# Kernel tuning notes

Hardware: AMD Instinct MI355X
Metric: run time of the kernel (lower is better)

The kernel has to match this reference:

```python
import jax, jax.numpy as jnp
import numpy as np

HEADS = 4
EPS_LN = 1e-6
EPS_IN = 1e-5


def _ln(x, g, b):
    m = x.mean(-1, keepdims=True)
    v = ((x - m) ** 2).mean(-1, keepdims=True)
    return (x - m) / jnp.sqrt(v + EPS_LN) * g + b


def _inorm(s):
    # nn.InstanceNorm2d(1) (affine=False): normalize each (batch, channel=head)
    # slice over the last two (N, N) dims, biased variance, eps=1e-5.
    m = s.mean((-2, -1), keepdims=True)
    v = ((s - m) ** 2).mean((-2, -1), keepdims=True)
    return (s - m) / jnp.sqrt(v + EPS_IN)


def setup_inputs() -> dict:
    key = jax.random.key(0)
    ks = jax.random.split(key, 32)
    B, C, Hh = 8, 256, HEADS
    sc = 1.0 / np.sqrt(C)

    def n(k, shape, s):
        return jax.random.normal(k, shape, jnp.float32) * s

    return {
        "x": n(ks[0], (B, C, 6, 6, 6), 1.0),
        # global branch params
        "g_tok_w": n(ks[1], (C,), 0.05), "g_tok_b": jnp.zeros((C,), jnp.float32),
        "g_ln1_g": jnp.ones((C,), jnp.float32), "g_ln1_b": jnp.zeros((C,), jnp.float32),
        "g_wq": n(ks[2], (C, C * Hh), sc), "g_wk": n(ks[3], (C, C * Hh), sc),
        "g_wv": n(ks[4], (C, C * Hh), sc), "g_wo": n(ks[5], (C * Hh, C), sc),
        "g_ln2_g": jnp.ones((C,), jnp.float32), "g_ln2_b": jnp.zeros((C,), jnp.float32),
        "g_mo_w": n(ks[6], (C, C), sc), "g_mo_b": jnp.zeros((C,), jnp.float32),
        # local branch params
        "l_pw": n(ks[7], (8, 8), 0.35), "l_pb": jnp.zeros((8,), jnp.float32),
        "l_ln1_g": jnp.ones((C,), jnp.float32), "l_ln1_b": jnp.zeros((C,), jnp.float32),
        "l_wq": n(ks[8], (C, C * Hh), sc), "l_wk": n(ks[9], (C, C * Hh), sc),
        "l_wv": n(ks[10], (C, C * Hh), sc), "l_wo": n(ks[11], (C * Hh, C), sc),
        "l_ln2_g": jnp.ones((C,), jnp.float32), "l_ln2_b": jnp.zeros((C,), jnp.float32),
        "l_mo_w": n(ks[12], (C, C), sc), "l_mo_b": jnp.zeros((C,), jnp.float32),
    }


def _global_branch(x, tok_w, tok_b, ln1_g, ln1_b, wq, wk, wv, wo, ln2_g, ln2_b, mo_w, mo_b):
    B, C, D, H, W = x.shape
    Hh = HEADS
    # TokenLearner_Global: conv1x1x1 (1->256) then mean over (D,H,W), then
    # view(B,C,C).mean(dim=1).  Since the conv is 1x1 on a single input channel,
    # this collapses exactly to: w * mean(x over C,D,H,W) + b.
    m = x.mean((1, 2, 3, 4))                       # (B,)
    tok = m[:, None] * tok_w + tok_b               # (B, C)
    res = tok
    t = _ln(tok, ln1_g, ln1_b)                     # (B, C)
    q = (t @ wq).reshape(B, Hh, C)                 # heads outer in the 1024 split
    k = (t @ wk).reshape(B, Hh, C)
    v = (t @ wv).reshape(B, Hh, C)
    # mh_q^T (B,h,C,1) @ mh_k (B,h,1,C) -> rank-1 (B,h,C,C) score map
    score = q[:, :, :, None] * k[:, :, None, :]
    a = jax.nn.softmax(_inorm(score), axis=-1)
    o = jnp.einsum('bhij,bhj->bhi', a, v)          # attn @ mh_v^T -> (B,h,C)
    # permute(0,3,2,1).view: flatten as (c, heads) with c outer
    o = o.transpose(0, 2, 1).reshape(B, C * Hh)
    out = o @ wo                                   # (B, C)
    tok2 = _ln(out + res, ln2_g, ln2_b)            # (B, C)
    # map_out conv1x1 + GELU on a spatially-constant expand -> compute once
    g = jax.nn.gelu(jnp.einsum('bc,oc->bo', tok2, mo_w) + mo_b, approximate=False)
    return jnp.broadcast_to(g[:, :, None, None, None], (B, C, D, H, W))


def _local_branch(x, pw, pb, ln1_g, ln1_b, wq, wk, wv, wo, ln2_g, ln2_b, mo_w, mo_b):
    B, C, D, H, W = x.shape
    Hh = HEADS
    # TokenLearner_Local: conv3d(1->8, k=2, s=2) per channel == patchify 2x2x2
    xp = x.reshape(B * C, 3, 2, 3, 2, 3, 2).transpose(0, 1, 3, 5, 2, 4, 6)
    xp = xp.reshape(B * C, 27, 8)                  # (BC, patches, patch_vol)
    tok = xp @ pw.T + pb                           # (BC, 27, 8) embed_dim=8
    tok = tok.reshape(B, C, 3, 3, 3, 2, 2, 2)
    # res: (b c)(d h w)(p1 p2 p3) -> b (d p1 h p2 w p3) c
    res = tok.transpose(0, 2, 5, 3, 6, 4, 7, 1).reshape(B, 216, C)
    # attn input: (b c)(d h w)(p1 p2 p3) -> (b d h w) (p1 p2 p3) c
    e = tok.reshape(B, C, 3, 3, 3, 8).transpose(0, 2, 3, 4, 5, 1).reshape(B * 27, 8, C)
    e = _ln(e, ln1_g, ln1_b)
    # (c heads) split: c outer, heads inner
    q = (e @ wq).reshape(B * 27, 8, C, Hh).transpose(0, 3, 2, 1)   # (B27,h,C,8)
    k = (e @ wk).reshape(B * 27, 8, C, Hh).transpose(0, 3, 1, 2)   # (B27,h,8,C)
    v = (e @ wv).reshape(B * 27, 8, C, Hh).transpose(0, 3, 2, 1)   # (B27,h,C,8)
    score = q @ k                                                  # (B27,h,C,C)
    a = jax.nn.softmax(_inorm(score), axis=-1)
    o = a @ v                                                      # (B27,h,C,8)
    # (b d h w) heads c (p1 p2 p3) -> b (d p1 h p2 w p3) (c heads)
    o = o.reshape(B, 3, 3, 3, Hh, C, 2, 2, 2)
    o = o.transpose(0, 1, 6, 2, 7, 3, 8, 5, 4).reshape(B, 216, C * Hh)
    out = o @ wo                                                   # (B,216,C)
    t2 = _ln(out + res, ln2_g, ln2_b)
    xm = t2.transpose(0, 2, 1).reshape(B, C, D, H, W)
    return jax.nn.gelu(
        jnp.einsum('bcdhw,oc->bodhw', xm, mo_w) + mo_b[None, :, None, None, None],
        approximate=False)


def reference(x,
              g_tok_w, g_tok_b, g_ln1_g, g_ln1_b, g_wq, g_wk, g_wv, g_wo,
              g_ln2_g, g_ln2_b, g_mo_w, g_mo_b,
              l_pw, l_pb, l_ln1_g, l_ln1_b, l_wq, l_wk, l_wv, l_wo,
              l_ln2_g, l_ln2_b, l_mo_w, l_mo_b):
    g = _global_branch(x, g_tok_w, g_tok_b, g_ln1_g, g_ln1_b, g_wq, g_wk, g_wv,
                       g_wo, g_ln2_g, g_ln2_b, g_mo_w, g_mo_b)
    l = _local_branch(x, l_pw, l_pb, l_ln1_g, l_ln1_b, l_wq, l_wk, l_wv,
                      l_wo, l_ln2_g, l_ln2_b, l_mo_w, l_mo_b)
    return x + g + l
```

## Files before the change

kernel.cpp:

```cpp
#include <hip/hip_runtime.h>
#include <stdint.h>
#include <math.h>

#define DEVFN __device__ __forceinline__
typedef unsigned short u16;
typedef short bf16x8 __attribute__((ext_vector_type(8)));
typedef float f32x4  __attribute__((ext_vector_type(4)));

DEVFN float blk_sum(float v, float* s4) {
  #pragma unroll
  for (int o = 32; o > 0; o >>= 1) v += __shfl_down(v, o, 64);
  __syncthreads();
  if ((threadIdx.x & 63) == 0) s4[threadIdx.x >> 6] = v;
  __syncthreads();
  return s4[0] + s4[1] + s4[2] + s4[3];
}

DEVFN float gelu_f(float x) {
  return 0.5f * x * (1.f + erff(x * 0.7071067811865475f));
}

DEVFN u16 bf16_rne(float f) {
  uint32_t u = __float_as_uint(f);
  return (u16)((u + 0x7fffu + ((u >> 16) & 1u)) >> 16);
}

DEVFN float bf2f(u16 v) { return __uint_as_float(((uint32_t)v) << 16); }

DEVFN void gload16(const u16* g, u16* l) {
  auto gp = (const __attribute__((address_space(1))) uint32_t*)(uintptr_t)g;
  auto lp = (__attribute__((address_space(3))) uint32_t*)(uintptr_t)l;
  __builtin_amdgcn_global_load_lds(gp, lp, 16, 0, 0);
}

DEVFN void trc_tile(const float* __restrict__ in, u16* __restrict__ out,
                    int R, int C, int r0, int c0, float (*tile)[33], int tid) {
  int tx = tid & 31, ty = tid >> 5;
  for (int i = ty; i < 32; i += 8) tile[i][tx] = in[(size_t)(r0 + i) * C + c0 + tx];
  __syncthreads();
  for (int i = ty; i < 32; i += 8)
    out[(size_t)(c0 + i) * R + r0 + tx] = bf16_rne(tile[tx][i]);
}

__global__ __launch_bounds__(256) void k_l_tok_prep(
    const float* __restrict__ x, const float* __restrict__ pw,
    const float* __restrict__ pb, const float* __restrict__ g1,
    const float* __restrict__ b1, float* __restrict__ res,
    u16* __restrict__ eln_bf, float* __restrict__ g_part,
    const float* __restrict__ wq, const float* __restrict__ wk,
    const float* __restrict__ wv, const float* __restrict__ wo,
    const float* __restrict__ mow, u16* __restrict__ WcatT,
    u16* __restrict__ woT, u16* __restrict__ moB) {
  __shared__ __align__(16) char smem[8448];
  int bid0 = blockIdx.x, tid = threadIdx.x;
  if (bid0 < 1728) {
    float* pws = (float*)smem;
    float* s4 = (float*)(smem + 256);
    int t = bid0;
    int b = t / 216, s = t % 216;
    int z = s / 36, y = (s / 6) % 6, xx = s % 6;
    int d = z >> 1, p1 = z & 1, hh = y >> 1, p2 = y & 1, ww = xx >> 1, p3 = xx & 1;
    int p = p1 * 4 + p2 * 2 + p3;
    int c = tid;
    if (c < 64) pws[c] = pw[c];
    __syncthreads();
    const float* xb = x + (b * 256 + c) * 216 + (2 * d) * 36 + (2 * hh) * 6 + 2 * ww;
    float v = pb[p];
    float xs = 0.f;
    #pragma unroll
    for (int q1 = 0; q1 < 2; ++q1)
      #pragma unroll
      for (int q2 = 0; q2 < 2; ++q2)
        #pragma unroll
        for (int q3 = 0; q3 < 2; ++q3) {
          float xv = xb[q1 * 36 + q2 * 6 + q3];
          xs += xv;
          v += xv * pws[p * 8 + (q1 * 4 + q2 * 2 + q3)];
        }
    float bs = blk_sum(xs, s4);
    if (c == 0) g_part[t] = bs;
    res[t * 256 + c] = v;
    float mu = blk_sum(v, s4) * (1.f / 256.f);
    float dd = v - mu;
    float var = blk_sum(dd * dd, s4) * (1.f / 256.f);
    eln_bf[t * 256 + c] = bf16_rne(dd * rsqrtf(var + 1e-6f) * g1[c] + b1[c]);
  } else {
    float (*tile)[33] = (float(*)[33])smem;
    int bid = bid0 - 1728;
    if (bid < 768) {
      int which = bid >> 8, b2 = bid & 255;
      const float* in = (which == 0) ? wq : (which == 1) ? wk : wv;
      u16* out = WcatT + which * 262144;
      int r0 = (b2 & 7) * 32, c0 = (b2 >> 3) * 32;
      trc_tile(in, out, 256, 1024, r0, c0, tile, tid);
    } else if (bid < 1024) {
      int b2 = bid - 768;
      int r0 = (b2 & 31) * 32, c0 = (b2 >> 5) * 32;
      trc_tile(wo, woT, 1024, 256, r0, c0, tile, tid);
    } else {
      int i = (bid - 1024) * 256 + tid;
      moB[i] = bf16_rne(mow[i]);
    }
  }
}

__global__ __launch_bounds__(256) void k_gemm_qkv_fused(
    const u16* __restrict__ A, const u16* __restrict__ BT, u16* __restrict__ C,
    const float* __restrict__ g_part, const float* __restrict__ tw_,
    const float* __restrict__ tb_, const float* __restrict__ g1,
    const float* __restrict__ b1, const float* __restrict__ wq,
    const float* __restrict__ wk, const float* __restrict__ wv,
    float* __restrict__ gqkv) {
  __shared__ __align__(16) char smem[16640];
  int bid = blockIdx.x, tid = threadIdx.x;
  if (bid < 1296) {
    const int N = 3072, K = 256;
    u16* aL = (u16*)smem;
    u16* bL = (u16*)smem + 2048;
    int rowblk = (bid % 27) * 64, colblk = (bid / 27) * 64;
    int lane = tid & 63, w = tid >> 6;
    int wr = (w >> 1) * 32, wc = (w & 1) * 32;
    int fm = lane & 15, lg = lane >> 4;
    f32x4 acc[2][2] = {};
    for (int kt = 0; kt < K; kt += 32) {
      __syncthreads();
      gload16(&A[(size_t)(rowblk + lane) * K + kt + w * 8], aL + w * 512);
      gload16(&BT[(size_t)(colblk + lane) * K + kt + w * 8], bL + w * 512);
      __syncthreads();
      bf16x8 bn[2];
      #pragma unroll
      for (int ni = 0; ni < 2; ++ni)
        bn[ni] = *(const bf16x8*)&bL[lg * 512 + (wc + ni * 16 + fm) * 8];
      #pragma unroll
      for (int mi = 0; mi < 2; ++mi) {
        bf16x8 af = *(const bf16x8*)&aL[lg * 512 + (wr + mi * 16 + fm) * 8];
        #pragma unroll
        for (int ni = 0; ni < 2; ++ni)
          acc[mi][ni] = __builtin_amdgcn_mfma_f32_16x16x32_bf16(af, bn[ni], acc[mi][ni], 0, 0, 0);
      }
    }
    int crow0 = rowblk + wr + lg * 4;
    int ccol  = colblk + wc + fm;
    #pragma unroll
    for (int mi = 0; mi < 2; ++mi)
      #pragma unroll
      for (int ni = 0; ni < 2; ++ni)
        #pragma unroll
        for (int r = 0; r < 4; ++r)
          C[(size_t)(crow0 + mi * 16 + r) * N + ccol + ni * 16] = bf16_rne(acc[mi][ni][r]);
  } else {
    float* ts = (float*)smem;
    float (*red)[4][8] = (float(*)[4][8])(smem + 8192);
    float* s4 = (float*)(smem + 16384);
    float* m_s = (float*)(smem + 16400);
    int rb = bid - 1296;
    float tw = tw_[tid], tb = tb_[tid], gg = g1[tid], bb = b1[tid];
    float S1 = blk_sum(tw, s4);
    float S2 = blk_sum(tw * tw, s4);
    float S3 = blk_sum(tb, s4);
    float S4 = blk_sum(tb * tb, s4);
    float S5 = blk_sum(tw * tb, s4);
    {
      int b = tid >> 5, sl = tid & 31;
      float a = 0.f;
      for (int k = sl; k < 216; k += 32) a += g_part[b * 216 + k];
      #pragma unroll
      for (int o = 16; o > 0; o >>= 1) a += __shfl_down(a, o, 32);
      if (sl == 0) m_s[b] = a * (1.f / 442368.f);
    }
    __syncthreads();
    #pragma unroll
    for (int b = 0; b < 8; ++b) {
      float m = m_s[b];
      float mu = (m * S1 + S3) * (1.f / 256.f);
      float var = (m * m * S2 + 2.f * m * S5 + S4) * (1.f / 256.f) - mu * mu;
      ts[b * 256 + tid] = (m * tw + tb - mu) * rsqrtf(var + 1e-6f) * gg + bb;
    }
    __syncthreads();
    int col0 = rb * 64;
    int cl = tid & 63, kq = tid >> 6;
    int col = col0 + cl;
    int m = col >> 10, cc = col & 1023;
    const float* W = (m == 0) ? wq : (m == 1) ? wk : wv;
    float acc[8] = {};
    for (int c = kq * 64; c < kq * 64 + 64; ++c) {
      float w = W[c * 1024 + cc];
      #pragma unroll
      for (int b = 0; b < 8; ++b) acc[b] = fmaf(ts[b * 256 + c], w, acc[b]);
    }
    #pragma unroll
    for (int b = 0; b < 8; ++b) red[cl][kq][b] = acc[b];
    __syncthreads();
    if (kq == 0) {
      #pragma unroll
      for (int b = 0; b < 8; ++b)
        gqkv[b * 3072 + col] = red[cl][0][b] + red[cl][1][b] + red[cl][2][b] + red[cl][3][b];
    }
  }
}

__global__ __launch_bounds__(256) void k_l_attn_fused(
    const u16* __restrict__ qkv, u16* __restrict__ o_buf,
    const float* __restrict__ gq, float* __restrict__ g_o) {
  __shared__ __align__(16) uint4 Qb[256], Kb[256];
  __shared__ __align__(16) u16 vt[16][264];
  __shared__ __align__(16) u16 Pl[256][72];
  __shared__ float rqA[64][4], rkA[64][4], rlq[64][4], rlk[64][4], s_ab[2];
  int bid = blockIdx.x, tid = threadIdx.x;
  if (bid >= 864) {
    float* ks = (float*)Qb;
    float* vs = ks + 256;
    float* s4 = (float*)Kb;
    int idx = bid - 864;
    int b = idx >> 2, h = idx & 3;
    int i = tid;
    const float* base = gq + b * 3072 + h * 256;
    float q = base[i];
    float k = base[1024 + i];
    ks[i] = k;
    vs[i] = base[2048 + i];
    float sq  = blk_sum(q, s4);
    float sq2 = blk_sum(q * q, s4);
    float sk  = blk_sum(k, s4);
    float sk2 = blk_sum(k * k, s4);
    float tot  = sq * sk * (1.f / 65536.f);
    float tot2 = sq2 * sk2 * (1.f / 65536.f);
    float rstd = rsqrtf(tot2 - tot * tot + 1e-5f);
    float A = rstd, B = -tot * rstd;
    float den = 0.f, num = 0.f;
    for (int j = 0; j < 256; ++j) {
      float w = __expf(fmaf(q * ks[j], A, B));
      den += w; num += w * vs[j];
    }
    g_o[b * 1024 + (i << 2) + h] = num / den;
    return;
  }
  int n = bid >> 2, h = bid & 3;
  int b = n / 27, patch = n % 27;
  int bz = 2 * (patch / 9), by = 2 * ((patch / 3) % 3), bx = 2 * (patch % 3);
  {
    int c = tid;
    u16 qv[8], kv[8], vv[8];
    #pragma unroll
    for (int p = 0; p < 8; ++p) {
      int t_l = b * 216 + (bz + (p >> 2)) * 36 + (by + ((p >> 1) & 1)) * 6 + (bx + (p & 1));
      const u16* row = qkv + (size_t)t_l * 3072 + (c << 2) + h;
      qv[p] = row[0]; kv[p] = row[1024]; vv[p] = row[2048];
    }
    uint32_t qw[4], kw[4];
    #pragma unroll
    for (int i = 0; i < 4; ++i) {
      qw[i] = (uint32_t)qv[2 * i] | ((uint32_t)qv[2 * i + 1] << 16);
      kw[i] = (uint32_t)kv[2 * i] | ((uint32_t)kv[2 * i + 1] << 16);
    }
    Qb[c] = make_uint4(qw[0], qw[1], qw[2], qw[3]);
    Kb[c] = make_uint4(kw[0], kw[1], kw[2], kw[3]);
    #pragma unroll
    for (int p = 0; p < 8; ++p) vt[p][c] = vv[p];
    vt[8][c] = 0x3F80u;
    #pragma unroll
    for (int r2 = 9; r2 < 16; ++r2) vt[r2][c] = 0;
  }
  __syncthreads();
  {
    int p = tid & 63, chunk = tid >> 6;
    int d = p >> 3, e = p & 7;
    float aq = 0.f, ak = 0.f, lq = 0.f, lk = 0.f;
    for (int cc = chunk * 64; cc < chunk * 64 + 64; ++cc) {
      const u16* qr = (const u16*)&Qb[cc];
      const u16* kr = (const u16*)&Kb[cc];
      float qd = bf2f(qr[d]), qe = bf2f(qr[e]);
      float kd = bf2f(kr[d]), ke = bf2f(kr[e]);
      aq = fmaf(qd, qe, aq); ak = fmaf(kd, ke, ak);
      if (e == 0) { lq += qd; lk += kd; }
    }
    rqA[p][chunk] = aq; rkA[p][chunk] = ak; rlq[p][chunk] = lq; rlk[p][chunk] = lk;
    __syncthreads();
    if (tid < 64) {
      float gq2 = rqA[tid][0] + rqA[tid][1] + rqA[tid][2] + rqA[tid][3];
      float gk = rkA[tid][0] + rkA[tid][1] + rkA[tid][2] + rkA[tid][3];
      float vprod = gq2 * gk, vmu = 0.f;
      if ((tid & 7) == 0) {
        float slq = rlq[tid][0] + rlq[tid][1] + rlq[tid][2] + rlq[tid][3];
        float slk = rlk[tid][0] + rlk[tid][1] + rlk[tid][2] + rlk[tid][3];
        vmu = slq * slk;
      }
      #pragma unroll
      for (int o = 32; o > 0; o >>= 1) {
        vprod += __shfl_down(vprod, o, 64);
        vmu   += __shfl_down(vmu, o, 64);
      }
      if (tid == 0) {
        float mu = vmu * (1.f / 65536.f), m2 = vprod * (1.f / 65536.f);
        float rstd = rsqrtf(m2 - mu * mu + 1e-5f);
        s_ab[0] = rstd; s_ab[1] = -mu * rstd;
      }
    }
    __syncthreads();
  }
  float Af = s_ab[0], Bf = s_ab[1];
  int lane = tid & 63, w = tid >> 6;
  int l15 = lane & 15, lg = lane >> 4;
  bf16x8 qf[4];
  #pragma unroll
  for (int qt = 0; qt < 4; ++qt)
    qf[qt] = *(const bf16x8*)&Qb[w * 64 + qt * 16 + l15];
  f32x4 acc_o[4] = {};
  #pragma unroll 1
  for (int jc = 0; jc < 4; ++jc) {
    bf16x8 kf[4];
    #pragma unroll
    for (int jt = 0; jt < 4; ++jt) {
      bf16x8 z = {};
      if (lg == 0) z = *(const bf16x8*)&Kb[jc * 64 + jt * 16 + l15];
      kf[jt] = z;
    }
    #pragma unroll
    for (int jt = 0; jt < 4; ++jt) {
      #pragma unroll
      for (int qt = 0; qt < 4; ++qt) {
        f32x4 zc = {};
        f32x4 s = __builtin_amdgcn_mfma_f32_16x16x32_bf16(kf[jt], qf[qt], zc, 0, 0, 0);
        float e0 = __expf(fmaf(s[0], Af, Bf));
        float e1 = __expf(fmaf(s[1], Af, Bf));
        float e2 = __expf(fmaf(s[2], Af, Bf));
        float e3 = __expf(fmaf(s[3], Af, Bf));
        uint32_t w0 = (__float_as_uint(e0) >> 16) | (__float_as_uint(e1) & 0xFFFF0000u);
        uint32_t w1 = (__float_as_uint(e2) >> 16) | (__float_as_uint(e3) & 0xFFFF0000u);
        int q = w * 64 + qt * 16 + l15;
        *(uint2*)&Pl[q][jt * 16 + lg * 4] = make_uint2(w0, w1);
      }
    }
    #pragma unroll
    for (int ks2 = 0; ks2 < 2; ++ks2) {
      bf16x8 vf = *(const bf16x8*)&vt[l15][jc * 64 + ks2 * 32 + lg * 8];
      #pragma unroll
      for (int qt = 0; qt < 4; ++qt) {
        bf16x8 pf = *(const bf16x8*)&Pl[w * 64 + qt * 16 + l15][ks2 * 32 + lg * 8];
        acc_o[qt] = __builtin_amdgcn_mfma_f32_16x16x32_bf16(pf, vf, acc_o[qt], 0, 0, 0);
      }
    }
  }
  int src = ((lane & 48) + 8) << 2;
  int p = l15;
  int t_l = b * 216 + (bz + (p >> 2)) * 36 + (by + ((p >> 1) & 1)) * 6 + (bx + (p & 1));
  #pragma unroll
  for (int qt = 0; qt < 4; ++qt) {
    #pragma unroll
    for (int r = 0; r < 4; ++r) {
      float den = __int_as_float(__builtin_amdgcn_ds_bpermute(src, __float_as_int(acc_o[qt][r])));
      if (p < 8) {
        int q = w * 64 + qt * 16 + lg * 4 + r;
        o_buf[(size_t)t_l * 1024 + (q << 2) + h] = bf16_rne(acc_o[qt][r] / den);
      }
    }
  }
}

__global__ __launch_bounds__(256) void k_gemm_sk_fused(
    const u16* __restrict__ A, const u16* __restrict__ BT, float* __restrict__ Cp,
    const float* __restrict__ g_o, const float* __restrict__ wo,
    float* __restrict__ part) {
  __shared__ __align__(16) char smem[8192];
  int bid = blockIdx.x, tid = threadIdx.x;
  if (bid < 216) {
    const int M = 1728, N = 256, K = 1024;
    u16* aL = (u16*)smem;
    u16* bL = (u16*)smem + 2048;
    int rowblk = (bid % 27) * 64, colblk = ((bid / 27) & 3) * 64;
    int kz = bid / 108, khalf = K >> 1;
    float* C = Cp + (size_t)kz * M * N;
    int lane = tid & 63, w = tid >> 6;
    int wr = (w >> 1) * 32, wc = (w & 1) * 32;
    int fm = lane & 15, lg = lane >> 4;
    f32x4 acc[2][2] = {};
    for (int kt = kz * khalf; kt < (kz + 1) * khalf; kt += 32) {
      __syncthreads();
      gload16(&A[(size_t)(rowblk + lane) * K + kt + w * 8], aL + w * 512);
      gload16(&BT[(size_t)(colblk + lane) * K + kt + w * 8], bL + w * 512);
      __syncthreads();
      bf16x8 bn[2];
      #pragma unroll
      for (int ni = 0; ni < 2; ++ni)
        bn[ni] = *(const bf16x8*)&bL[lg * 512 + (wc + ni * 16 + fm) * 8];
      #pragma unroll
      for (int mi = 0; mi < 2; ++mi) {
        bf16x8 af = *(const bf16x8*)&aL[lg * 512 + (wr + mi * 16 + fm) * 8];
        #pragma unroll
        for (int ni = 0; ni < 2; ++ni)
          acc[mi][ni] = __builtin_amdgcn_mfma_f32_16x16x32_bf16(af, bn[ni], acc[mi][ni], 0, 0, 0);
      }
    }
    int crow0 = rowblk + wr + lg * 4;
    int ccol  = colblk + wc + fm;
    #pragma unroll
    for (int mi = 0; mi < 2; ++mi)
      #pragma unroll
      for (int ni = 0; ni < 2; ++ni)
        #pragma unroll
        for (int r = 0; r < 4; ++r)
          C[(size_t)(crow0 + mi * 16 + r) * N + ccol + ni * 16] = acc[mi][ni][r];
  } else {
    float* os = (float*)smem;
    int kc = bid - 216;
    os[tid] = g_o[(tid >> 5) * 1024 + kc * 32 + (tid & 31)];
    __syncthreads();
    float acc[8] = {};
    #pragma unroll
    for (int kk = 0; kk < 32; ++kk) {
      float w = wo[(size_t)(kc * 32 + kk) * 256 + tid];
      #pragma unroll
      for (int b = 0; b < 8; ++b) acc[b] = fmaf(os[b * 32 + kk], w, acc[b]);
    }
    #pragma unroll
    for (int b = 0; b < 8; ++b) part[kc * 2048 + b * 256 + tid] = acc[b];
  }
}

__global__ __launch_bounds__(256) void k_l_ln2_fused(
    const float* __restrict__ proj0, const float* __restrict__ proj1,
    const float* __restrict__ res, const float* __restrict__ g2,
    const float* __restrict__ b2, u16* __restrict__ t2b,
    const float* __restrict__ part, const float* __restrict__ g_part,
    const float* __restrict__ tw_, const float* __restrict__ tb_,
    const float* __restrict__ gg2, const float* __restrict__ gb2,
    float* __restrict__ t2g) {
  __shared__ float s4[4];
  int bid = blockIdx.x, c = threadIdx.x;
  if (bid < 1728) {
    int t = bid;
    float v = proj0[t * 256 + c] + proj1[t * 256 + c] + res[t * 256 + c];
    float mu = blk_sum(v, s4) * (1.f / 256.f);
    float d = v - mu;
    float var = blk_sum(d * d, s4) * (1.f / 256.f);
    t2b[t * 256 + c] = bf16_rne(d * rsqrtf(var + 1e-6f) * g2[c] + b2[c]);
  } else {
    int b = bid - 1728;
    float a = (c < 216) ? g_part[b * 216 + c] : 0.f;
    float m = blk_sum(a, s4) * (1.f / 442368.f);
    float v = m * tw_[c] + tb_[c];
    #pragma unroll
    for (int kc = 0; kc < 32; ++kc) v += part[kc * 2048 + b * 256 + c];
    float mu = blk_sum(v, s4) * (1.f / 256.f);
    float d = v - mu;
    float var = blk_sum(d * d, s4) * (1.f / 256.f);
    t2g[b * 256 + c] = d * rsqrtf(var + 1e-6f) * gg2[c] + gb2[c];
  }
}

__global__ __launch_bounds__(256) void k_g_mo(
    const float* __restrict__ t2g, const float* __restrict__ mow,
    const float* __restrict__ mob, float* __restrict__ g_vec) {
  __shared__ float ts[2048];
  int tid = threadIdx.x;
  for (int i = tid; i < 2048; i += 256) ts[i] = t2g[i];
  __syncthreads();
  int ol = tid >> 5, cs = tid & 31;
  int o = blockIdx.x * 8 + ol;
  const float* wrow = mow + (size_t)o * 256;
  float acc[8] = {};
  #pragma unroll
  for (int i = 0; i < 8; ++i) {
    float w = wrow[i * 32 + cs];
    #pragma unroll
    for (int b = 0; b < 8; ++b) acc[b] = fmaf(ts[b * 256 + i * 32 + cs], w, acc[b]);
  }
  #pragma unroll
  for (int b = 0; b < 8; ++b) {
    float v = acc[b];
    #pragma unroll
    for (int off = 16; off > 0; off >>= 1) v += __shfl_down(v, off, 32);
    if (cs == 0) g_vec[b * 256 + o] = gelu_f(v + mob[o]);
  }
}

__global__ __launch_bounds__(256) void k_gemm_mo_final(
    const u16* __restrict__ A, const u16* __restrict__ BT,
    const float* __restrict__ x, const float* __restrict__ gvec,
    const float* __restrict__ mob, float* __restrict__ out) {
  __shared__ __align__(16) char smem[16640];
  u16* aL = (u16*)smem;
  u16* bL = (u16*)smem + 2048;
  float (*ct)[65] = (float(*)[65])smem;
  const int K = 256;
  int tid = threadIdx.x;
  int rowblk = blockIdx.x * 64, colblk = blockIdx.y * 64;
  int lane = tid & 63, w = tid >> 6;
  int wr = (w >> 1) * 32, wc = (w & 1) * 32;
  int fm = lane & 15, lg = lane >> 4;
  f32x4 acc[2][2] = {};
  for (int kt = 0; kt < K; kt += 32) {
    __syncthreads();
    gload16(&A[(size_t)(rowblk + lane) * K + kt + w * 8], aL + w * 512);
    gload16(&BT[(size_t)(colblk + lane) * K + kt + w * 8], bL + w * 512);
    __syncthreads();
    bf16x8 bn[2];
    #pragma unroll
    for (int ni = 0; ni < 2; ++ni)
      bn[ni] = *(const bf16x8*)&bL[lg * 512 + (wc + ni * 16 + fm) * 8];
    #pragma unroll
    for (int mi = 0; mi < 2; ++mi) {
      bf16x8 af = *(const bf16x8*)&aL[lg * 512 + (wr + mi * 16 + fm) * 8];
      #pragma unroll
      for (int ni = 0; ni < 2; ++ni)
        acc[mi][ni] = __builtin_amdgcn_mfma_f32_16x16x32_bf16(af, bn[ni], acc[mi][ni], 0, 0, 0);
    }
  }
  __syncthreads();
  int row_l0 = wr + lg * 4;
  #pragma unroll
  for (int mi = 0; mi < 2; ++mi)
    #pragma unroll
    for (int ni = 0; ni < 2; ++ni)
      #pragma unroll
      for (int r = 0; r < 4; ++r)
        ct[row_l0 + mi * 16 + r][wc + ni * 16 + fm] = acc[mi][ni][r];
  __syncthreads();
  int s_l = tid & 63;
  #pragma unroll 4
  for (int pass = 0; pass < 16; ++pass) {
    int col_l = (tid >> 6) * 16 + pass;
    int row = rowblk + s_l, col = colblk + col_l;
    int b = row / 216, s = row - b * 216;
    size_t idx = (size_t)b * 55296 + (size_t)col * 216 + s;
    out[idx] = x[idx] + gvec[b * 256 + col] + gelu_f(ct[s_l][col_l] + mob[col]);
  }
}

extern "C" void kernel_launch(void* const* d_in, const int* in_sizes, int n_in,
                              void* d_out, int out_size, void* d_ws, size_t ws_size,
                              hipStream_t stream) {
  const float* x     = (const float*)d_in[0];
  const float* g_tw  = (const float*)d_in[1];
  const float* g_tb  = (const float*)d_in[2];
  const float* g_l1g = (const float*)d_in[3];
  const float* g_l1b = (const float*)d_in[4];
  const float* g_wq  = (const float*)d_in[5];
  const float* g_wk  = (const float*)d_in[6];
  const float* g_wv  = (const float*)d_in[7];
  const float* g_wo  = (const float*)d_in[8];
  const float* g_l2g = (const float*)d_in[9];
  const float* g_l2b = (const float*)d_in[10];
  const float* g_mow = (const float*)d_in[11];
  const float* g_mob = (const float*)d_in[12];
  const float* l_pw  = (const float*)d_in[13];
  const float* l_pb  = (const float*)d_in[14];
  const float* l_l1g = (const float*)d_in[15];
  const float* l_l1b = (const float*)d_in[16];
  const float* l_wq  = (const float*)d_in[17];
  const float* l_wk  = (const float*)d_in[18];
  const float* l_wv  = (const float*)d_in[19];
  const float* l_wo  = (const float*)d_in[20];
  const float* l_l2g = (const float*)d_in[21];
  const float* l_l2b = (const float*)d_in[22];
  const float* l_mow = (const float*)d_in[23];
  const float* l_mob = (const float*)d_in[24];
  float* out = (float*)d_out;
  float* ws  = (float*)d_ws;

  float* g_qkv  = ws + 4096;
  float* g_o    = ws + 28672;
  float* g_vec  = ws + 36864;
  float* g_part = ws + 38912;
  float* res    = ws + 40960;
  u16*   eln_bf = (u16*)(ws + 483328);
  u16*   WcatT  = (u16*)(ws + 704512);
  u16*   woT    = (u16*)(ws + 1097728);
  u16*   moB    = (u16*)(ws + 1228800);
  u16*   qkvb   = (u16*)(ws + 1261568);
  u16*   o_buf  = (u16*)(ws + 6569984);
  float* proj   = ws + 7454720;
  u16*   t2b    = (u16*)(ws + 8339456);
  float* part_wo= ws + 8560640;
  float* t2g    = ws + 8626176;

  k_l_tok_prep<<<3008, 256, 0, stream>>>(x, l_pw, l_pb, l_l1g, l_l1b,
                                         res, eln_bf, g_part,
                                         l_wq, l_wk, l_wv, l_wo, l_mow,
                                         WcatT, woT, moB);
  k_gemm_qkv_fused<<<1344, 256, 0, stream>>>(eln_bf, WcatT, qkvb,
                                             g_part, g_tw, g_tb, g_l1g, g_l1b,
                                             g_wq, g_wk, g_wv, g_qkv);
  k_l_attn_fused<<<896, 256, 0, stream>>>(qkvb, o_buf, g_qkv, g_o);
  k_gemm_sk_fused<<<248, 256, 0, stream>>>(o_buf, woT, proj, g_o, g_wo, part_wo);
  k_l_ln2_fused<<<1736, 256, 0, stream>>>(proj, proj + 442368, res,
                                          l_l2g, l_l2b, t2b,
                                          part_wo, g_part, g_tw, g_tb,
                                          g_l2g, g_l2b, t2g);
  k_g_mo<<<32, 256, 0, stream>>>(t2g, g_mow, g_mob, g_vec);
  k_gemm_mo_final<<<dim3(27, 4), 256, 0, stream>>>(t2b, moB, x, g_vec, l_mob, out);
}
```

Before: 108.5 us.

## Stage full-K GEMM tiles into XOR-swizzled LDS and vectorize output stores

```diff
diff --git a/kernel.cpp b/kernel.cpp
--- a/kernel.cpp
+++ b/kernel.cpp
@@ -31,6 +31,19 @@
   auto gp = (const __attribute__((address_space(1))) uint32_t*)(uintptr_t)g;
   auto lp = (__attribute__((address_space(3))) uint32_t*)(uintptr_t)l;
   __builtin_amdgcn_global_load_lds(gp, lp, 16, 0, 0);
+}
+
+DEVFN void stage64x256(const u16* G, size_t gstride, u16* L, int w, int lane) {
+  #pragma unroll
+  for (int i = 0; i < 8; ++i) {
+    int row = w * 16 + 2 * i + (lane >> 5);
+    int c16 = (lane & 31) ^ (row & 7);
+    gload16(G + (size_t)row * gstride + c16 * 8, L + (w * 16 + 2 * i) * 256);
+  }
+}
+
+DEVFN bf16x8 lread(const u16* L, int row, int k16) {
+  return *(const bf16x8*)&L[row * 256 + ((k16 ^ (row & 7)) << 3)];
 }
 
 DEVFN void trc_tile(const float* __restrict__ in, u16* __restrict__ out,
@@ -111,43 +124,48 @@
     const float* __restrict__ b1, const float* __restrict__ wq,
     const float* __restrict__ wk, const float* __restrict__ wv,
     float* __restrict__ gqkv) {
-  __shared__ __align__(16) char smem[16640];
+  __shared__ __align__(16) char smem[65536];
   int bid = blockIdx.x, tid = threadIdx.x;
   if (bid < 1296) {
     const int N = 3072, K = 256;
     u16* aL = (u16*)smem;
-    u16* bL = (u16*)smem + 2048;
+    u16* bL = (u16*)smem + 16384;
     int rowblk = (bid % 27) * 64, colblk = (bid / 27) * 64;
     int lane = tid & 63, w = tid >> 6;
     int wr = (w >> 1) * 32, wc = (w & 1) * 32;
     int fm = lane & 15, lg = lane >> 4;
+    stage64x256(A + (size_t)rowblk * K, K, aL, w, lane);
+    stage64x256(BT + (size_t)colblk * K, K, bL, w, lane);
+    __syncthreads();
     f32x4 acc[2][2] = {};
-    for (int kt = 0; kt < K; kt += 32) {
-      __syncthreads();
-      gload16(&A[(size_t)(rowblk + lane) * K + kt + w * 8], aL + w * 512);
-      gload16(&BT[(size_t)(colblk + lane) * K + kt + w * 8], bL + w * 512);
-      __syncthreads();
-      bf16x8 bn[2];
-      #pragma unroll
-      for (int ni = 0; ni < 2; ++ni)
-        bn[ni] = *(const bf16x8*)&bL[lg * 512 + (wc + ni * 16 + fm) * 8];
-      #pragma unroll
-      for (int mi = 0; mi < 2; ++mi) {
-        bf16x8 af = *(const bf16x8*)&aL[lg * 512 + (wr + mi * 16 + fm) * 8];
-        #pragma unroll
-        for (int ni = 0; ni < 2; ++ni)
-          acc[mi][ni] = __builtin_amdgcn_mfma_f32_16x16x32_bf16(af, bn[ni], acc[mi][ni], 0, 0, 0);
-      }
-    }
-    int crow0 = rowblk + wr + lg * 4;
-    int ccol  = colblk + wc + fm;
+    #pragma unroll
+    for (int kk = 0; kk < 8; ++kk) {
+      int k16 = kk * 4 + lg;
+      bf16x8 bn0 = lread(bL, wc + fm, k16);
+      bf16x8 bn1 = lread(bL, wc + 16 + fm, k16);
+      bf16x8 af0 = lread(aL, wr + fm, k16);
+      bf16x8 af1 = lread(aL, wr + 16 + fm, k16);
+      acc[0][0] = __builtin_amdgcn_mfma_f32_16x16x32_bf16(af0, bn0, acc[0][0], 0, 0, 0);
+      acc[0][1] = __builtin_amdgcn_mfma_f32_16x16x32_bf16(af0, bn1, acc[0][1], 0, 0, 0);
+      acc[1][0] = __builtin_amdgcn_mfma_f32_16x16x32_bf16(af1, bn0, acc[1][0], 0, 0, 0);
+      acc[1][1] = __builtin_amdgcn_mfma_f32_16x16x32_bf16(af1, bn1, acc[1][1], 0, 0, 0);
+    }
+    __syncthreads();
+    u16* ct = (u16*)smem;
     #pragma unroll
     for (int mi = 0; mi < 2; ++mi)
       #pragma unroll
       for (int ni = 0; ni < 2; ++ni)
         #pragma unroll
         for (int r = 0; r < 4; ++r)
-          C[(size_t)(crow0 + mi * 16 + r) * N + ccol + ni * 16] = bf16_rne(acc[mi][ni][r]);
+          ct[(wr + mi * 16 + lg * 4 + r) * 64 + wc + ni * 16 + fm] = bf16_rne(acc[mi][ni][r]);
+    __syncthreads();
+    #pragma unroll
+    for (int pass = 0; pass < 2; ++pass) {
+      int id = pass * 256 + tid;
+      int r = id >> 3, u = id & 7;
+      *(uint4*)&C[(size_t)(rowblk + r) * N + colblk + u * 8] = *(uint4*)&ct[r * 64 + u * 8];
+    }
   } else {
     float* ts = (float*)smem;
     float (*red)[4][8] = (float(*)[4][8])(smem + 8192);
@@ -238,8 +256,9 @@
   int n = bid >> 2, h = bid & 3;
   int b = n / 27, patch = n % 27;
   int bz = 2 * (patch / 9), by = 2 * ((patch / 3) % 3), bx = 2 * (patch % 3);
+  int tid2 = tid;
   {
-    int c = tid;
+    int c = tid2;
     u16 qv[8], kv[8], vv[8];
     #pragma unroll
     for (int p = 0; p < 8; ++p) {
@@ -263,7 +282,7 @@
   }
   __syncthreads();
   {
-    int p = tid & 63, chunk = tid >> 6;
+    int p = tid2 & 63, chunk = tid2 >> 6;
     int d = p >> 3, e = p & 7;
     float aq = 0.f, ak = 0.f, lq = 0.f, lk = 0.f;
     for (int cc = chunk * 64; cc < chunk * 64 + 64; ++cc) {
@@ -276,13 +295,13 @@
     }
     rqA[p][chunk] = aq; rkA[p][chunk] = ak; rlq[p][chunk] = lq; rlk[p][chunk] = lk;
     __syncthreads();
-    if (tid < 64) {
-      float gq2 = rqA[tid][0] + rqA[tid][1] + rqA[tid][2] + rqA[tid][3];
-      float gk = rkA[tid][0] + rkA[tid][1] + rkA[tid][2] + rkA[tid][3];
+    if (tid2 < 64) {
+      float gq2 = rqA[tid2][0] + rqA[tid2][1] + rqA[tid2][2] + rqA[tid2][3];
+      float gk = rkA[tid2][0] + rkA[tid2][1] + rkA[tid2][2] + rkA[tid2][3];
       float vprod = gq2 * gk, vmu = 0.f;
-      if ((tid & 7) == 0) {
-        float slq = rlq[tid][0] + rlq[tid][1] + rlq[tid][2] + rlq[tid][3];
-        float slk = rlk[tid][0] + rlk[tid][1] + rlk[tid][2] + rlk[tid][3];
+      if ((tid2 & 7) == 0) {
+        float slq = rlq[tid2][0] + rlq[tid2][1] + rlq[tid2][2] + rlq[tid2][3];
+        float slk = rlk[tid2][0] + rlk[tid2][1] + rlk[tid2][2] + rlk[tid2][3];
         vmu = slq * slk;
       }
       #pragma unroll
@@ -290,7 +309,7 @@
         vprod += __shfl_down(vprod, o, 64);
         vmu   += __shfl_down(vmu, o, 64);
       }
-      if (tid == 0) {
+      if (tid2 == 0) {
         float mu = vmu * (1.f / 65536.f), m2 = vprod * (1.f / 65536.f);
         float rstd = rsqrtf(m2 - mu * mu + 1e-5f);
         s_ab[0] = rstd; s_ab[1] = -mu * rstd;
@@ -299,7 +318,7 @@
     __syncthreads();
   }
   float Af = s_ab[0], Bf = s_ab[1];
-  int lane = tid & 63, w = tid >> 6;
+  int lane = tid2 & 63, w = tid2 >> 6;
   int l15 = lane & 15, lg = lane >> 4;
   bf16x8 qf[4];
   #pragma unroll
@@ -361,45 +380,55 @@
     const u16* __restrict__ A, const u16* __restrict__ BT, float* __restrict__ Cp,
     const float* __restrict__ g_o, const float* __restrict__ wo,
     float* __restrict__ part) {
-  __shared__ __align__(16) char smem[8192];
+  __shared__ __align__(16) char smem[65536];
   int bid = blockIdx.x, tid = threadIdx.x;
   if (bid < 216) {
     const int M = 1728, N = 256, K = 1024;
     u16* aL = (u16*)smem;
-    u16* bL = (u16*)smem + 2048;
+    u16* bL = (u16*)smem + 16384;
     int rowblk = (bid % 27) * 64, colblk = ((bid / 27) & 3) * 64;
-    int kz = bid / 108, khalf = K >> 1;
+    int kz = bid / 108;
     float* C = Cp + (size_t)kz * M * N;
     int lane = tid & 63, w = tid >> 6;
     int wr = (w >> 1) * 32, wc = (w & 1) * 32;
     int fm = lane & 15, lg = lane >> 4;
     f32x4 acc[2][2] = {};
-    for (int kt = kz * khalf; kt < (kz + 1) * khalf; kt += 32) {
+    #pragma unroll 1
+    for (int step = 0; step < 2; ++step) {
+      int kt = kz * 512 + step * 256;
       __syncthreads();
-      gload16(&A[(size_t)(rowblk + lane) * K + kt + w * 8], aL + w * 512);
-      gload16(&BT[(size_t)(colblk + lane) * K + kt + w * 8], bL + w * 512);
+      stage64x256(A + (size_t)rowblk * K + kt, K, aL, w, lane);
+      stage64x256(BT + (size_t)colblk * K + kt, K, bL, w, lane);
       __syncthreads();
-      bf16x8 bn[2];
-      #pragma unroll
-      for (int ni = 0; ni < 2; ++ni)
-        bn[ni] = *(const bf16x8*)&bL[lg * 512 + (wc + ni * 16 + fm) * 8];
-      #pragma unroll
-      for (int mi = 0; mi < 2; ++mi) {
-        bf16x8 af = *(const bf16x8*)&aL[lg * 512 + (wr + mi * 16 + fm) * 8];
-        #pragma unroll
-        for (int ni = 0; ni < 2; ++ni)
-          acc[mi][ni] = __builtin_amdgcn_mfma_f32_16x16x32_bf16(af, bn[ni], acc[mi][ni], 0, 0, 0);
+      #pragma unroll
+      for (int kk = 0; kk < 8; ++kk) {
+        int k16 = kk * 4 + lg;
+        bf16x8 bn0 = lread(bL, wc + fm, k16);
+        bf16x8 bn1 = lread(bL, wc + 16 + fm, k16);
+        bf16x8 af0 = lread(aL, wr + fm, k16);
+        bf16x8 af1 = lread(aL, wr + 16 + fm, k16);
+        acc[0][0] = __builtin_amdgcn_mfma_f32_16x16x32_bf16(af0, bn0, acc[0][0], 0, 0, 0);
+        acc[0][1] = __builtin_amdgcn_mfma_f32_16x16x32_bf16(af0, bn1, acc[0][1], 0, 0, 0);
+        acc[1][0] = __builtin_amdgcn_mfma_f32_16x16x32_bf16(af1, bn0, acc[1][0], 0, 0, 0);
+        acc[1][1] = __builtin_amdgcn_mfma_f32_16x16x32_bf16(af1, bn1, acc[1][1], 0, 0, 0);
       }
     }
-    int crow0 = rowblk + wr + lg * 4;
-    int ccol  = colblk + wc + fm;
+    __syncthreads();
+    float* ct = (float*)smem;
     #pragma unroll
     for (int mi = 0; mi < 2; ++mi)
       #pragma unroll
       for (int ni = 0; ni < 2; ++ni)
         #pragma unroll
         for (int r = 0; r < 4; ++r)
-          C[(size_t)(crow0 + mi * 16 + r) * N + ccol + ni * 16] = acc[mi][ni][r];
+          ct[(wr + mi * 16 + lg * 4 + r) * 64 + wc + ni * 16 + fm] = acc[mi][ni][r];
+    __syncthreads();
+    #pragma unroll
+    for (int pass = 0; pass < 4; ++pass) {
+      int id = pass * 256 + tid;
+      int r = id >> 4, u = id & 15;
+      *(float4*)&C[(size_t)(rowblk + r) * N + colblk + u * 4] = *(float4*)&ct[r * 64 + u * 4];
+    }
   } else {
     float* os = (float*)smem;
     int kc = bid - 216;
@@ -478,9 +507,9 @@
     const u16* __restrict__ A, const u16* __restrict__ BT,
     const float* __restrict__ x, const float* __restrict__ gvec,
     const float* __restrict__ mob, float* __restrict__ out) {
-  __shared__ __align__(16) char smem[16640];
+  __shared__ __align__(16) char smem[65536];
   u16* aL = (u16*)smem;
-  u16* bL = (u16*)smem + 2048;
+  u16* bL = (u16*)smem + 16384;
   float (*ct)[65] = (float(*)[65])smem;
   const int K = 256;
   int tid = threadIdx.x;
@@ -488,23 +517,21 @@
   int lane = tid & 63, w = tid >> 6;
   int wr = (w >> 1) * 32, wc = (w & 1) * 32;
   int fm = lane & 15, lg = lane >> 4;
+  stage64x256(A + (size_t)rowblk * K, K, aL, w, lane);
+  stage64x256(BT + (size_t)colblk * K, K, bL, w, lane);
+  __syncthreads();
   f32x4 acc[2][2] = {};
-  for (int kt = 0; kt < K; kt += 32) {
-    __syncthreads();
-    gload16(&A[(size_t)(rowblk + lane) * K + kt + w * 8], aL + w * 512);
-    gload16(&BT[(size_t)(colblk + lane) * K + kt + w * 8], bL + w * 512);
-    __syncthreads();
-    bf16x8 bn[2];
-    #pragma unroll
-    for (int ni = 0; ni < 2; ++ni)
-      bn[ni] = *(const bf16x8*)&bL[lg * 512 + (wc + ni * 16 + fm) * 8];
-    #pragma unroll
-    for (int mi = 0; mi < 2; ++mi) {
-      bf16x8 af = *(const bf16x8*)&aL[lg * 512 + (wr + mi * 16 + fm) * 8];
-      #pragma unroll
-      for (int ni = 0; ni < 2; ++ni)
-        acc[mi][ni] = __builtin_amdgcn_mfma_f32_16x16x32_bf16(af, bn[ni], acc[mi][ni], 0, 0, 0);
-    }
+  #pragma unroll
+  for (int kk = 0; kk < 8; ++kk) {
+    int k16 = kk * 4 + lg;
+    bf16x8 bn0 = lread(bL, wc + fm, k16);
+    bf16x8 bn1 = lread(bL, wc + 16 + fm, k16);
+    bf16x8 af0 = lread(aL, wr + fm, k16);
+    bf16x8 af1 = lread(aL, wr + 16 + fm, k16);
+    acc[0][0] = __builtin_amdgcn_mfma_f32_16x16x32_bf16(af0, bn0, acc[0][0], 0, 0, 0);
+    acc[0][1] = __builtin_amdgcn_mfma_f32_16x16x32_bf16(af0, bn1, acc[0][1], 0, 0, 0);
+    acc[1][0] = __builtin_amdgcn_mfma_f32_16x16x32_bf16(af1, bn0, acc[1][0], 0, 0, 0);
+    acc[1][1] = __builtin_amdgcn_mfma_f32_16x16x32_bf16(af1, bn1, acc[1][1], 0, 0, 0);
   }
   __syncthreads();
   int row_l0 = wr + lg * 4;
```

Result: faster. 99.78 us (-8.0%).
